# Kernel tuning notes

Measured on AMD Instinct MI355X. Metric: run time of the kernel, lower is better.

The kernel has to match this reference:

```python
import jax, jax.numpy as jnp
import numpy as np
import itertools

EPS = 1e-6
OUT = 1024            # out_size[0]
RRNG = (16.0, 16.0)   # local sampling region per column (rrange)


def setup_inputs() -> dict:
    key = jax.random.key(0)
    ks = jax.random.split(key, 6)
    b, n, c, g, rad, rank = 8, 4096, 32, 4, 4, 2
    k = n // c
    in_size = 1024
    rng = jnp.array([float(OUT), float(in_size)])
    # continuous index tuples, strictly inside [0, dim-1)
    means = jax.random.uniform(ks[0], (b, n, rank)) * (rng - 1.0)
    sigmas = jax.random.uniform(ks[1], (b, n, rank)) * 0.5 + 0.1
    values = jax.random.normal(ks[2], (b, n))
    x = jax.random.normal(ks[3], (b, in_size))
    sampled_u = jax.random.uniform(ks[4], (b, k, c, g, rank))
    rr_u = jax.random.uniform(ks[5], (b, k, c, rad, rank))
    return {"x": x, "means": means, "sigmas": sigmas, "values": values,
            "sampled_u": sampled_u, "rr_u": rr_u}


def _generate_integer_tuples(means, sampled_u, rr_u, rng, rrng):
    # means: (b,k,c,rank)
    b, k, c, rank = means.shape
    # floor/ceil combinatorics: itertools.product([True, False], repeat=rank)
    fm = jnp.asarray([[int(v) for v in bits]
                      for bits in itertools.product([True, False], repeat=rank)],
                     dtype=bool)                       # (2^rank, rank)
    m = means[:, :, :, None, :]                         # (b,k,c,1,rank)
    neighbor = jnp.where(fm[None, None, None], jnp.floor(m), jnp.ceil(m))
    neighbor = jnp.broadcast_to(neighbor, (b, k, c, 2 ** rank, rank)).astype(jnp.int32)
    # global uniform samples over the full index range
    sampled = jnp.floor(sampled_u * (1.0 - EPS) * rng).astype(jnp.int32)
    # local uniform samples in a window of size rrng around round(means)
    mns = jnp.round(means)[:, :, :, None, :]
    lower = mns - rrng * 0.5
    upper = mns + rrng * 0.5
    lower = jnp.where(lower < 0.0, 0.0, lower)
    lower = jnp.where(upper > rng, rng - rrng, lower)
    rr = jnp.floor(rr_u * (1.0 - EPS) * rrng + lower).astype(jnp.int32)
    allints = jnp.concatenate([neighbor, sampled, rr], axis=3)  # (b,k,c,L,rank)
    return allints.reshape(b, k, -1, rank)                      # l = c*L


def _densities(points, means, sigmas):
    # points: (b,k,l,rank)  means/sigmas: (b,k,c,rank) -> (b,k,l,c)
    inv = jnp.sqrt(1.0 / (EPS + sigmas))
    diff = (points[:, :, :, None, :] - means[:, :, None, :, :]) * inv[:, :, None, :, :]
    return jnp.exp(-0.5 * jnp.sum(diff * diff, axis=-1))


def _mark_dups(ids):
    # ids: (b,k,l) scalar-encoded tuples; True = later occurrence of a duplicate
    # within the same (b,k) chunk context. Stable sort keeps first occurrence.
    order = jnp.argsort(ids, axis=-1)
    s = jnp.take_along_axis(ids, order, axis=-1)
    dup_s = jnp.concatenate([jnp.zeros(s.shape[:-1] + (1,), dtype=bool),
                             s[..., 1:] == s[..., :-1]], axis=-1)
    inv = jnp.argsort(order, axis=-1)
    return jnp.take_along_axis(dup_s, inv, axis=-1)


def reference(x, means, sigmas, values, sampled_u, rr_u):
    b, n, rank = means.shape
    _, k, c, g, _ = sampled_u.shape
    in_size = x.shape[1]
    rng = jnp.array([OUT, in_size], dtype=x.dtype)
    rrng = jnp.array(RRNG, dtype=x.dtype)

    means = means.reshape(b, k, c, rank)
    sigmas = sigmas.reshape(b, k, c, rank)
    values = values.reshape(b, k, c)

    ints = _generate_integer_tuples(means, sampled_u, rr_u, rng, rrng)  # (b,k,l,rank)
    indfl = ints.astype(x.dtype)

    dups = _mark_dups(ints[..., 0] * in_size + ints[..., 1])            # (b,k,l)
    props = _densities(indfl, means, sigmas)                            # (b,k,l,c)
    props = jnp.where(dups[..., None], 0.0, props)
    props = props / jnp.sum(props, axis=2, keepdims=True)

    vals = jnp.sum(props * values[:, :, None, :], axis=3)               # (b,k,l)

    idx = ints.reshape(b, -1, rank)
    v = vals.reshape(b, -1)
    bidx = jnp.arange(b)[:, None]
    # sparse contraction: out[b, i0] += v * x[b, i1]
    contrib = v * x[bidx, idx[..., 1]]
    out = jnp.zeros((b, OUT), x.dtype).at[bidx, idx[..., 0]].add(contrib)
    return out
```

## Files before the change

### kernel.cpp

```cpp
#include <hip/hip_runtime.h>

#define CQ 32
#define KQ 128
#define OUTN 1024
#define BQ 8
#define NACC (BQ * OUTN)
#define HSZ 1024
#define PPL 6
#define WPB 4
#define NGROUP (BQ * KQ)
#define NBLK (NGROUP / WPB)
#define WS_NEED ((size_t)NGROUP * OUTN * sizeof(float))

__global__ void zero_out(float* __restrict__ out) {
    int i = blockIdx.x * blockDim.x + threadIdx.x;
    if (i < NACC) out[i] = 0.0f;
}

__device__ __forceinline__ float wave_red_dpp(float v) {
#define DPPADD(ctrl)                                                              \
    {                                                                             \
        int t_ = __builtin_amdgcn_update_dpp(0, __float_as_int(v), (ctrl), 0xF,   \
                                             0xF, true);                          \
        v += __int_as_float(t_);                                                  \
    }
    DPPADD(0x111)
    DPPADD(0x112)
    DPPADD(0x114)
    DPPADD(0x118)
    DPPADD(0x142)
    DPPADD(0x143)
#undef DPPADD
    return v;
}

__global__ __launch_bounds__(WPB * 64) void sparse_wave(
    const float* __restrict__ x,
    const float* __restrict__ means,
    const float* __restrict__ sigmas,
    const float* __restrict__ values,
    const float* __restrict__ su,
    const float* __restrict__ ru,
    float* __restrict__ dst,
    int use_ws)
{
    const int lane = threadIdx.x & 63;
    const int w = threadIdx.x >> 6;
    const int gk = blockIdx.x * WPB + w;
    const int b = gk >> 7;
    const float CEPS = (float)(1.0 - 1e-6);

    __shared__ int htab[WPB][HSZ];
    __shared__ float acc[WPB][OUTN];

    #pragma unroll
    for (int i = 0; i < HSZ / 64; ++i) htab[w][i * 64 + lane] = -1;
    if (use_ws) {
        #pragma unroll
        for (int i = 0; i < OUTN / 64; ++i) acc[w][i * 64 + lane] = 0.0f;
    }

    float pm0 = 0.f, pm1 = 0.f, pi0 = 0.f, pi1 = 0.f, pv = 0.f;
    if (lane < CQ) {
        int cb = gk * CQ + lane;
        float2 mg = *(const float2*)&means[cb * 2];
        float2 sg = *(const float2*)&sigmas[cb * 2];
        pm0 = mg.x; pm1 = mg.y;
        pi0 = __fsqrt_rn(__fdiv_rn(1.0f, __fadd_rn(1e-6f, sg.x)));
        pi1 = __fsqrt_rn(__fdiv_rn(1.0f, __fadd_rn(1e-6f, sg.y)));
        pv  = values[cb];
    }

    int p0[PPL], p1[PPL];
    #pragma unroll
    for (int i = 0; i < PPL; ++i) {
        const int pt = i * 64 + lane;
        const int c = pt / 12, j = pt % 12;
        const float mm0 = __shfl(pm0, c), mm1 = __shfl(pm1, c);
        int q0, q1;
        if (j < 4) {
            q0 = (int)((j >= 2) ? ceilf(mm0) : floorf(mm0));
            q1 = (int)((j & 1) ? ceilf(mm1) : floorf(mm1));
        } else if (j < 8) {
            float2 uu = *(const float2*)&su[(gk * CQ + c) * 8 + (j - 4) * 2];
            q0 = (int)floorf(__fmul_rn(__fmul_rn(uu.x, CEPS), 1024.0f));
            q1 = (int)floorf(__fmul_rn(__fmul_rn(uu.y, CEPS), 1024.0f));
        } else {
            float2 uu = *(const float2*)&ru[(gk * CQ + c) * 8 + (j - 8) * 2];
            float mn0 = rintf(mm0), mn1 = rintf(mm1);
            float lo0 = mn0 - 8.0f; if (lo0 < 0.0f) lo0 = 0.0f; if (mn0 + 8.0f > 1024.0f) lo0 = 1008.0f;
            float lo1 = mn1 - 8.0f; if (lo1 < 0.0f) lo1 = 0.0f; if (mn1 + 8.0f > 1024.0f) lo1 = 1008.0f;
            q0 = (int)floorf(__fadd_rn(__fmul_rn(__fmul_rn(uu.x, CEPS), 16.0f), lo0));
            q1 = (int)floorf(__fadd_rn(__fmul_rn(__fmul_rn(uu.y, CEPS), 16.0f), lo1));
        }
        p0[i] = q0; p1[i] = q1;
    }

    float xv[PPL];
    #pragma unroll
    for (int i = 0; i < PPL; ++i) {
        int g1 = p1[i] < 0 ? 0 : (p1[i] > OUTN - 1 ? OUTN - 1 : p1[i]);
        xv[i] = x[b * OUTN + g1];
    }

    unsigned dupm = 0u;
    #pragma unroll
    for (int i = 0; i < PPL; ++i) {
        const int myid = p0[i] * 1024 + p1[i];
        int slot = (int)(((unsigned)myid * 2654435761u) >> 22);
        while (true) {
            int prev = atomicCAS(&htab[w][slot], -1, myid);
            if (prev == -1) break;
            if (prev == myid) { dupm |= (1u << i); break; }
            slot = (slot + 1) & (HSZ - 1);
        }
    }

    const float pf0[PPL] = {(float)p0[0], (float)p0[1], (float)p0[2],
                            (float)p0[3], (float)p0[4], (float)p0[5]};
    const float pf1[PPL] = {(float)p1[0], (float)p1[1], (float)p1[2],
                            (float)p1[3], (float)p1[4], (float)p1[5]};

    float vals[PPL] = {0.f, 0.f, 0.f, 0.f, 0.f, 0.f};
    #pragma unroll
    for (int cc = 0; cc < CQ; ++cc) {
        const float m0 = __shfl(pm0, cc), m1 = __shfl(pm1, cc);
        const float i0 = __shfl(pi0, cc), i1 = __shfl(pi1, cc);
        const float vv = __shfl(pv, cc);
        float e[PPL];
        float s = 0.f;
        #pragma unroll
        for (int i = 0; i < PPL; ++i) {
            float d0 = (pf0[i] - m0) * i0;
            float d1 = (pf1[i] - m1) * i1;
            float t = __expf(-0.5f * (d0 * d0 + d1 * d1));
            t = ((dupm >> i) & 1u) ? 0.0f : t;
            e[i] = t; s += t;
        }
        s = wave_red_dpp(s);
        const float ss = __shfl(s, 63);
        const float wn = vv / ss;
        #pragma unroll
        for (int i = 0; i < PPL; ++i) vals[i] += e[i] * wn;
    }

    #pragma unroll
    for (int i = 0; i < PPL; ++i) {
        if (!((dupm >> i) & 1u) && p0[i] >= 0 && p0[i] < OUTN) {
            float contrib = vals[i] * xv[i];
            if (use_ws) atomicAdd(&acc[w][p0[i]], contrib);
            else        atomicAdd(&dst[b * OUTN + p0[i]], contrib);
        }
    }

    if (use_ws) {
        float* wsp = dst + (size_t)gk * OUTN;
        #pragma unroll
        for (int ii = 0; ii < OUTN / 256; ++ii) {
            int idx = ii * 256 + lane * 4;
            float4 v = *(const float4*)&acc[w][idx];
            *(float4*)&wsp[idx] = v;
        }
    }
}

__global__ void reduce_ws(const float* __restrict__ ws, float* __restrict__ out) {
    int t = blockIdx.x * blockDim.x + threadIdx.x;
    if (t >= NACC) return;
    int b = t >> 10, cidx = t & (OUTN - 1);
    const float* p = ws + (size_t)b * KQ * OUTN + cidx;
    float s0 = 0.0f, s1 = 0.0f, s2 = 0.0f, s3 = 0.0f;
    #pragma unroll
    for (int k = 0; k < KQ; k += 4) {
        s0 += p[(size_t)(k + 0) * OUTN];
        s1 += p[(size_t)(k + 1) * OUTN];
        s2 += p[(size_t)(k + 2) * OUTN];
        s3 += p[(size_t)(k + 3) * OUTN];
    }
    out[t] = (s0 + s1) + (s2 + s3);
}

extern "C" void kernel_launch(void* const* d_in, const int* in_sizes, int n_in,
                              void* d_out, int out_size, void* d_ws, size_t ws_size,
                              hipStream_t stream) {
    const float* x      = (const float*)d_in[0];
    const float* means  = (const float*)d_in[1];
    const float* sigmas = (const float*)d_in[2];
    const float* values = (const float*)d_in[3];
    const float* su     = (const float*)d_in[4];
    const float* ru     = (const float*)d_in[5];
    float* out = (float*)d_out;
    float* ws  = (float*)d_ws;

    if (ws_size >= WS_NEED) {
        sparse_wave<<<dim3(NBLK), dim3(WPB * 64), 0, stream>>>(
            x, means, sigmas, values, su, ru, ws, 1);
        reduce_ws<<<dim3((NACC + 127) / 128), dim3(128), 0, stream>>>(ws, out);
    } else {
        zero_out<<<dim3((NACC + 255) / 256), dim3(256), 0, stream>>>(out);
        sparse_wave<<<dim3(NBLK), dim3(WPB * 64), 0, stream>>>(
            x, means, sigmas, values, su, ru, out, 0);
    }
}
```

Before: 90.49 us.

## Split each k-group across two cooperating waves with shared hash and accumulator

New measurement: 86.42 us. 4.5% less time.

```diff
diff --git a/kernel.cpp b/kernel.cpp
--- a/kernel.cpp
+++ b/kernel.cpp
@@ -6,10 +6,9 @@
 #define BQ 8
 #define NACC (BQ * OUTN)
 #define HSZ 1024
-#define PPL 6
-#define WPB 4
+#define PPW 3
+#define WPG 2
 #define NGROUP (BQ * KQ)
-#define NBLK (NGROUP / WPB)
 #define WS_NEED ((size_t)NGROUP * OUTN * sizeof(float))
 
 __global__ void zero_out(float* __restrict__ out) {
@@ -34,7 +33,7 @@
     return v;
 }
 
-__global__ __launch_bounds__(WPB * 64) void sparse_wave(
+__global__ __launch_bounds__(WPG * 64, 2) void sparse_wave(
     const float* __restrict__ x,
     const float* __restrict__ means,
     const float* __restrict__ sigmas,
@@ -44,20 +43,22 @@
     float* __restrict__ dst,
     int use_ws)
 {
-    const int lane = threadIdx.x & 63;
-    const int w = threadIdx.x >> 6;
-    const int gk = blockIdx.x * WPB + w;
+    const int tid = threadIdx.x;
+    const int lane = tid & 63;
+    const int w = tid >> 6;
+    const int gk = blockIdx.x;
     const int b = gk >> 7;
     const float CEPS = (float)(1.0 - 1e-6);
 
-    __shared__ int htab[WPB][HSZ];
-    __shared__ float acc[WPB][OUTN];
-
-    #pragma unroll
-    for (int i = 0; i < HSZ / 64; ++i) htab[w][i * 64 + lane] = -1;
+    __shared__ __align__(16) int htab[HSZ];
+    __shared__ __align__(16) float acc[OUTN];
+    __shared__ float spart[WPG][CQ];
+
+    #pragma unroll
+    for (int i = 0; i < HSZ / 128; ++i) htab[i * 128 + tid] = -1;
     if (use_ws) {
         #pragma unroll
-        for (int i = 0; i < OUTN / 64; ++i) acc[w][i * 64 + lane] = 0.0f;
+        for (int i = 0; i < OUTN / 128; ++i) acc[i * 128 + tid] = 0.0f;
     }
 
     float pm0 = 0.f, pm1 = 0.f, pi0 = 0.f, pi1 = 0.f, pv = 0.f;
@@ -71,10 +72,10 @@
         pv  = values[cb];
     }
 
-    int p0[PPL], p1[PPL];
-    #pragma unroll
-    for (int i = 0; i < PPL; ++i) {
-        const int pt = i * 64 + lane;
+    int p0[PPW], p1[PPW];
+    #pragma unroll
+    for (int i = 0; i < PPW; ++i) {
+        const int pt = w * 192 + i * 64 + lane;
         const int c = pt / 12, j = pt % 12;
         const float mm0 = __shfl(pm0, c), mm1 = __shfl(pm1, c);
         int q0, q1;
@@ -96,69 +97,75 @@
         p0[i] = q0; p1[i] = q1;
     }
 
-    float xv[PPL];
-    #pragma unroll
-    for (int i = 0; i < PPL; ++i) {
+    float xv[PPW];
+    #pragma unroll
+    for (int i = 0; i < PPW; ++i) {
         int g1 = p1[i] < 0 ? 0 : (p1[i] > OUTN - 1 ? OUTN - 1 : p1[i]);
         xv[i] = x[b * OUTN + g1];
     }
 
+    __syncthreads();
+
     unsigned dupm = 0u;
     #pragma unroll
-    for (int i = 0; i < PPL; ++i) {
+    for (int i = 0; i < PPW; ++i) {
         const int myid = p0[i] * 1024 + p1[i];
         int slot = (int)(((unsigned)myid * 2654435761u) >> 22);
         while (true) {
-            int prev = atomicCAS(&htab[w][slot], -1, myid);
+            int prev = atomicCAS(&htab[slot], -1, myid);
             if (prev == -1) break;
             if (prev == myid) { dupm |= (1u << i); break; }
             slot = (slot + 1) & (HSZ - 1);
         }
     }
 
-    const float pf0[PPL] = {(float)p0[0], (float)p0[1], (float)p0[2],
-                            (float)p0[3], (float)p0[4], (float)p0[5]};
-    const float pf1[PPL] = {(float)p1[0], (float)p1[1], (float)p1[2],
-                            (float)p1[3], (float)p1[4], (float)p1[5]};
-
-    float vals[PPL] = {0.f, 0.f, 0.f, 0.f, 0.f, 0.f};
+    const float pf0[PPW] = {(float)p0[0], (float)p0[1], (float)p0[2]};
+    const float pf1[PPW] = {(float)p1[0], (float)p1[1], (float)p1[2]};
+
+    float e[CQ][PPW];
     #pragma unroll
     for (int cc = 0; cc < CQ; ++cc) {
         const float m0 = __shfl(pm0, cc), m1 = __shfl(pm1, cc);
         const float i0 = __shfl(pi0, cc), i1 = __shfl(pi1, cc);
-        const float vv = __shfl(pv, cc);
-        float e[PPL];
         float s = 0.f;
         #pragma unroll
-        for (int i = 0; i < PPL; ++i) {
+        for (int i = 0; i < PPW; ++i) {
             float d0 = (pf0[i] - m0) * i0;
             float d1 = (pf1[i] - m1) * i1;
             float t = __expf(-0.5f * (d0 * d0 + d1 * d1));
             t = ((dupm >> i) & 1u) ? 0.0f : t;
-            e[i] = t; s += t;
+            e[cc][i] = t; s += t;
         }
         s = wave_red_dpp(s);
-        const float ss = __shfl(s, 63);
-        const float wn = vv / ss;
-        #pragma unroll
-        for (int i = 0; i < PPL; ++i) vals[i] += e[i] * wn;
-    }
-
-    #pragma unroll
-    for (int i = 0; i < PPL; ++i) {
+        if (lane == 63) spart[w][cc] = s;
+    }
+    __syncthreads();
+
+    float vals[PPW] = {0.f, 0.f, 0.f};
+    #pragma unroll
+    for (int cc = 0; cc < CQ; ++cc) {
+        const float ss = spart[0][cc] + spart[1][cc];
+        const float wn = __shfl(pv, cc) / ss;
+        #pragma unroll
+        for (int i = 0; i < PPW; ++i) vals[i] += e[cc][i] * wn;
+    }
+
+    #pragma unroll
+    for (int i = 0; i < PPW; ++i) {
         if (!((dupm >> i) & 1u) && p0[i] >= 0 && p0[i] < OUTN) {
             float contrib = vals[i] * xv[i];
-            if (use_ws) atomicAdd(&acc[w][p0[i]], contrib);
+            if (use_ws) atomicAdd(&acc[p0[i]], contrib);
             else        atomicAdd(&dst[b * OUTN + p0[i]], contrib);
         }
     }
 
     if (use_ws) {
+        __syncthreads();
         float* wsp = dst + (size_t)gk * OUTN;
         #pragma unroll
-        for (int ii = 0; ii < OUTN / 256; ++ii) {
-            int idx = ii * 256 + lane * 4;
-            float4 v = *(const float4*)&acc[w][idx];
+        for (int ii = 0; ii < OUTN / (128 * 4); ++ii) {
+            int idx = ii * 512 + tid * 4;
+            float4 v = *(const float4*)&acc[idx];
             *(float4*)&wsp[idx] = v;
         }
     }
@@ -193,12 +200,12 @@
     float* ws  = (float*)d_ws;
 
     if (ws_size >= WS_NEED) {
-        sparse_wave<<<dim3(NBLK), dim3(WPB * 64), 0, stream>>>(
+        sparse_wave<<<dim3(NGROUP), dim3(WPG * 64), 0, stream>>>(
             x, means, sigmas, values, su, ru, ws, 1);
         reduce_ws<<<dim3((NACC + 127) / 128), dim3(128), 0, stream>>>(ws, out);
     } else {
         zero_out<<<dim3((NACC + 255) / 256), dim3(256), 0, stream>>>(out);
-        sparse_wave<<<dim3(NBLK), dim3(WPB * 64), 0, stream>>>(
+        sparse_wave<<<dim3(NGROUP), dim3(WPG * 64), 0, stream>>>(
             x, means, sigmas, values, su, ru, out, 0);
     }
 }
```
